# Performance work log

Hardware: AMD Instinct MI355X
Metric: run time of the kernel (lower is better)

## Reference

```python
import jax, jax.numpy as jnp
import numpy as np

K = 5          # number of spline bins
B = 5.0        # tail bound
HIDDEN = 8
MIN_W = 1e-3; MIN_H = 1e-3; MIN_D = 1e-3  # RQS defaults (Durkan et al.)


def setup_inputs() -> dict:
    n, d = 32768, 64
    L = d - 1
    P = 3 * K - 1
    ks = jax.random.split(jax.random.key(0), 8)
    x = jax.random.normal(ks[0], (n, d), jnp.float32) * 2.0
    init_param = jax.random.uniform(ks[1], (P,), jnp.float32, -0.5, 0.5)
    # ragged first layers: layer l (predicts dim l+1) sees x[:, :l+1]; zero-pad to width L
    mask = (jnp.arange(L)[None, :] <= jnp.arange(L)[:, None]).astype(jnp.float32)
    W1 = jax.random.normal(ks[2], (L, L, HIDDEN), jnp.float32) * 0.2 * mask[:, :, None]
    b1 = jax.random.normal(ks[3], (L, HIDDEN), jnp.float32) * 0.1
    W2 = jax.random.normal(ks[4], (L, HIDDEN, HIDDEN), jnp.float32) * 0.2
    b2 = jax.random.normal(ks[5], (L, HIDDEN), jnp.float32) * 0.1
    W3 = jax.random.normal(ks[6], (L, HIDDEN, P), jnp.float32) * 0.2
    b3 = jax.random.normal(ks[7], (L, P), jnp.float32) * 0.1
    return {"x": x, "init_param": init_param, "W1": W1, "b1": b1,
            "W2": W2, "b2": b2, "W3": W3, "b3": b3}


def _rqs(xf, Wu, Hu, Du):
    # xf: (M,), Wu/Hu: (M,K), Du: (M,K-1) -- vectorized unconstrained RQS, forward
    inside = (xf >= -B) & (xf <= B)
    const = float(np.log(np.exp(1.0 - MIN_D) - 1.0))
    Dpad = jnp.pad(Du, ((0, 0), (1, 1)), constant_values=const)

    widths = MIN_W + (1.0 - MIN_W * K) * jax.nn.softmax(Wu, axis=-1)
    cumw = jnp.pad(jnp.cumsum(widths, -1), ((0, 0), (1, 0)))
    cumw = 2.0 * B * cumw - B
    cumw = cumw.at[:, 0].set(-B).at[:, -1].set(B)
    widths = cumw[:, 1:] - cumw[:, :-1]

    heights = MIN_H + (1.0 - MIN_H * K) * jax.nn.softmax(Hu, axis=-1)
    cumh = jnp.pad(jnp.cumsum(heights, -1), ((0, 0), (1, 0)))
    cumh = 2.0 * B * cumh - B
    cumh = cumh.at[:, 0].set(-B).at[:, -1].set(B)
    heights = cumh[:, 1:] - cumh[:, :-1]

    derivs = MIN_D + jax.nn.softplus(Dpad)  # (M, K+1)

    xc = jnp.clip(xf, -B, B)
    idx = jnp.clip(jnp.sum(xc[:, None] >= cumw, axis=-1) - 1, 0, K - 1)
    take = lambda a: jnp.take_along_axis(a, idx[:, None], axis=-1)[:, 0]

    icw, ibw = take(cumw), take(widths)
    ich, ih = take(cumh), take(heights)
    idl = take(heights / widths)
    idv = take(derivs)
    idvp1 = take(derivs[:, 1:])

    theta = (xc - icw) / ibw
    tmt = theta * (1.0 - theta)
    num = ih * (idl * theta * theta + idv * tmt)
    den = idl + (idv + idvp1 - 2.0 * idl) * tmt
    out = ich + num / den
    dnum = idl * idl * (idvp1 * theta * theta + 2.0 * idl * tmt + idv * (1.0 - theta) ** 2)
    ld = jnp.log(dnum) - 2.0 * jnp.log(den)
    return jnp.where(inside, out, xf), jnp.where(inside, ld, 0.0)


def reference(x, init_param, W1, b1, W2, b2, W3, b3):
    n, d = x.shape
    L = d - 1
    P = 3 * K - 1
    # mask re-applied so padded W1 entries are exactly inert (ragged Linear(i, hidden))
    mask = (jnp.arange(L)[None, :] <= jnp.arange(L)[:, None]).astype(x.dtype)
    h = jnp.tanh(jnp.einsum('nj,ljh->lnh', x[:, :L], W1 * mask[:, :, None]) + b1[:, None, :])
    h = jnp.tanh(jnp.einsum('lnh,lhg->lng', h, W2) + b2[:, None, :])
    out = jnp.einsum('lng,lgp->lnp', h, W3) + b3[:, None, :]      # (L, n, P)
    p0 = jnp.broadcast_to(init_param, (1, n, P))                  # dim 0 uses init_param
    params = jnp.concatenate([p0, out], axis=0).reshape(d * n, P)  # dim-major, matches Ws layout
    Wu, Hu, Du = params[:, :K], params[:, K:2 * K], params[:, 2 * K:]
    xf = x.T.reshape(-1)  # x.transpose(0,1).flatten()
    zs, lds = _rqs(xf, Wu, Hu, Du)
    # NOTE: faithfully replicates the original's reshape of the dim-major flat
    # vector directly to (n, d) (as in the torch source).
    return zs.reshape(n, d), lds.reshape(n, d).sum(axis=1)
```

## Files before the change

### kernel.cpp

```cpp
#include <hip/hip_runtime.h>
#include <hip/hip_bf16.h>
#include <math.h>

#define KK 5
#define Bc 5.0f
#define NN 32768
#define DD 64
#define LL 63
#define PP 14
#define MIN_Wc 0.001f
#define MIN_Hc 0.001f
#define MIN_Dc 0.001f

typedef float f4 __attribute__((ext_vector_type(4)));
typedef float f32x4 __attribute__((ext_vector_type(4)));
typedef short short8 __attribute__((ext_vector_type(8)));

__device__ __forceinline__ float rcp_fast(float v)  { return __builtin_amdgcn_rcpf(v); }
__device__ __forceinline__ float exp_fast(float v)  { return __expf(v); }
__device__ __forceinline__ float log_fast(float v)  { return __logf(v); }
__device__ __forceinline__ float tanh_fast(float v) {
    float e = exp_fast(2.0f * v);
    return 1.0f - 2.0f * rcp_fast(e + 1.0f);
}
__device__ __forceinline__ float softplus_fast(float v) {
    return (v > 15.0f) ? v : log_fast(1.0f + exp_fast(v));
}
__device__ __forceinline__ ushort to_bf16u(float v) {
    __hip_bfloat16 b = __float2bfloat16(v);
    return *(ushort*)&b;
}

__global__ __launch_bounds__(256) void pack_b1(const float* __restrict__ W1,
                                               ushort* __restrict__ Bp) {
    int id = blockIdx.x * 256 + threadIdx.x;
    int n = id >> 6, k = id & 63;
    float v = 0.f;
    if (n < 504 && k < 63) {
        int l = n >> 3, h = n & 7;
        v = W1[(l * 63 + k) * 8 + h];
    }
    Bp[id] = to_bf16u(v);
}

#define AS 72
__global__ __launch_bounds__(256) void mlp1_kernel(
    const float* __restrict__ x, const ushort* __restrict__ Bp,
    const float* __restrict__ b1, ushort* __restrict__ h1out)
{
    __shared__ ushort Alds[64 * AS];
    __shared__ ushort Blds[128 * AS];
    const int tid = threadIdx.x;
    const int row0 = blockIdx.x * 64;
    const int nbase = blockIdx.y * 128;

    {
        int r = tid >> 2, c4 = (tid & 3) * 16;
        const f4* xg = (const f4*)(x + (size_t)(row0 + r) * 64 + c4);
        #pragma unroll
        for (int i = 0; i < 4; ++i) {
            f4 v = xg[i];
            ushort4 u;
            u.x = to_bf16u(v.x); u.y = to_bf16u(v.y);
            u.z = to_bf16u(v.z); u.w = to_bf16u(v.w);
            *(ushort4*)(&Alds[r * AS + c4 + i * 4]) = u;
        }
    }
    {
        const short8* src = (const short8*)(Bp + (size_t)nbase * 64);
        #pragma unroll
        for (int i = 0; i < 4; ++i) {
            int e = tid * 4 + i;
            int n = e >> 3, kc = (e & 7) * 8;
            *(short8*)(&Blds[n * AS + kc]) = src[e];
        }
    }
    __syncthreads();

    const int lane = tid & 63, wave = tid >> 6;
    const int m0 = wave * 16;
    const int qg = lane >> 4;
    const int ln = lane & 15;

    short8 a0 = *(const short8*)(&Alds[(m0 + ln) * AS + qg * 8]);
    short8 a1 = *(const short8*)(&Alds[(m0 + ln) * AS + 32 + qg * 8]);

    #pragma unroll
    for (int t = 0; t < 8; ++t) {
        short8 bf0 = *(const short8*)(&Blds[(t * 16 + ln) * AS + qg * 8]);
        short8 bf1 = *(const short8*)(&Blds[(t * 16 + ln) * AS + 32 + qg * 8]);
        f32x4 acc = {0.f, 0.f, 0.f, 0.f};
        acc = __builtin_amdgcn_mfma_f32_16x16x32_bf16(a0, bf0, acc, 0, 0, 0);
        acc = __builtin_amdgcn_mfma_f32_16x16x32_bf16(a1, bf1, acc, 0, 0, 0);

        int ng = nbase + t * 16 + ln;
        bool valid = ng < 504;
        float bias = valid ? b1[ng] : 0.f;
        int l = ng >> 3, h = ng & 7;
        ushort* dst = h1out + ((size_t)l * NN + row0 + m0 + qg * 4) * 8 + h;
        #pragma unroll
        for (int r = 0; r < 4; ++r) {
            float v = tanh_fast(acc[r] + bias);
            if (valid) dst[r * 8] = to_bf16u(v);
        }
    }
}

__global__ __launch_bounds__(256) void spline_kernel(
    const float* __restrict__ x, const float* __restrict__ init_param,
    const ushort* __restrict__ h1g,
    const float* __restrict__ W2, const float* __restrict__ b2,
    const float* __restrict__ W3, const float* __restrict__ b3,
    float* __restrict__ out)
{
    __shared__ float xs[64 * 65];
    const int s0 = blockIdx.x * 64;
    const int tid = threadIdx.x;
    for (int q = tid; q < 64 * 64; q += 256) {
        int r = q >> 6, c = q & 63;
        xs[r * 65 + c] = x[(size_t)(s0 + r) * 64 + c];
    }
    __syncthreads();

    const int lane = tid & 63, wave = tid >> 6;
    const int t = blockIdx.y * 4 + wave;

    #pragma unroll 1
    for (int kk = 0; kk < 4; ++kk) {
        int dd = __builtin_amdgcn_readfirstlane(t + kk * 16);

        float p[PP];
        if (dd == 0) {
            #pragma unroll
            for (int i = 0; i < PP; ++i) p[i] = init_param[i];
        } else {
            const int l = dd - 1;
            const uint4* hp = (const uint4*)(h1g + (size_t)l * NN * 8);
            uint4 hv = hp[s0 + lane];
            float h1f[8];
            h1f[0] = __uint_as_float(hv.x << 16);
            h1f[1] = __uint_as_float(hv.x & 0xFFFF0000u);
            h1f[2] = __uint_as_float(hv.y << 16);
            h1f[3] = __uint_as_float(hv.y & 0xFFFF0000u);
            h1f[4] = __uint_as_float(hv.z << 16);
            h1f[5] = __uint_as_float(hv.z & 0xFFFF0000u);
            h1f[6] = __uint_as_float(hv.w << 16);
            h1f[7] = __uint_as_float(hv.w & 0xFFFF0000u);

            float h2[8];
            #pragma unroll
            for (int g = 0; g < 8; ++g) h2[g] = b2[l * 8 + g];
            #pragma unroll
            for (int h = 0; h < 8; ++h) {
                #pragma unroll
                for (int g = 0; g < 8; ++g)
                    h2[g] = fmaf(h1f[h], W2[l * 64 + h * 8 + g], h2[g]);
            }
            #pragma unroll
            for (int g = 0; g < 8; ++g) h2[g] = tanh_fast(h2[g]);

            #pragma unroll
            for (int q = 0; q < PP; ++q) p[q] = b3[l * PP + q];
            #pragma unroll
            for (int g = 0; g < 8; ++g) {
                #pragma unroll
                for (int q = 0; q < PP; ++q)
                    p[q] = fmaf(h2[g], W3[(l * 8 + g) * PP + q], p[q]);
            }
        }

        const float xf = xs[lane * 65 + dd];

        float wmax = p[0];
        #pragma unroll
        for (int i = 1; i < KK; ++i) wmax = fmaxf(wmax, p[i]);
        float we[KK]; float wsum = 0.f;
        #pragma unroll
        for (int i = 0; i < KK; ++i) { we[i] = exp_fast(p[i] - wmax); wsum += we[i]; }
        const float wnorm = (1.0f - MIN_Wc * KK) * rcp_fast(wsum);
        float cumw[KK + 1], wdt[KK];
        cumw[0] = -Bc;
        float acw = 0.f;
        #pragma unroll
        for (int i = 0; i < KK; ++i) { acw += MIN_Wc + wnorm * we[i]; cumw[i + 1] = 2.f * Bc * acw - Bc; }
        cumw[KK] = Bc;
        #pragma unroll
        for (int i = 0; i < KK; ++i) wdt[i] = cumw[i + 1] - cumw[i];

        float hmax = p[KK];
        #pragma unroll
        for (int i = 1; i < KK; ++i) hmax = fmaxf(hmax, p[KK + i]);
        float he[KK]; float hsum = 0.f;
        #pragma unroll
        for (int i = 0; i < KK; ++i) { he[i] = exp_fast(p[KK + i] - hmax); hsum += he[i]; }
        const float hnorm = (1.0f - MIN_Hc * KK) * rcp_fast(hsum);
        float cumh[KK + 1], hgt[KK];
        cumh[0] = -Bc;
        float ach = 0.f;
        #pragma unroll
        for (int i = 0; i < KK; ++i) { ach += MIN_Hc + hnorm * he[i]; cumh[i + 1] = 2.f * Bc * ach - Bc; }
        cumh[KK] = Bc;
        #pragma unroll
        for (int i = 0; i < KK; ++i) hgt[i] = cumh[i + 1] - cumh[i];

        float derivs[KK + 1];
        derivs[0] = 1.0f;
        derivs[KK] = 1.0f;
        #pragma unroll
        for (int i = 0; i < KK - 1; ++i) derivs[i + 1] = MIN_Dc + softplus_fast(p[2 * KK + i]);

        const float xc = fminf(fmaxf(xf, -Bc), Bc);

        float icw = cumw[0], ibw = wdt[0], ich = cumh[0], ih = hgt[0];
        float idv = derivs[0], idvp1 = derivs[1];
        #pragma unroll
        for (int i = 1; i < KK; ++i) {
            bool c = xc >= cumw[i];
            icw   = c ? cumw[i]       : icw;
            ibw   = c ? wdt[i]        : ibw;
            ich   = c ? cumh[i]       : ich;
            ih    = c ? hgt[i]        : ih;
            idv   = c ? derivs[i]     : idv;
            idvp1 = c ? derivs[i + 1] : idvp1;
        }

        const float ibw_r = rcp_fast(ibw);
        const float idl = ih * ibw_r;
        const float theta = (xc - icw) * ibw_r;
        const float omt = 1.0f - theta;
        const float tmt = theta * omt;
        const float num = ih * (idl * theta * theta + idv * tmt);
        const float den = idl + (idv + idvp1 - 2.0f * idl) * tmt;
        const float outv = ich + num * rcp_fast(den);
        const float dnum = idl * idl * (idvp1 * theta * theta + 2.0f * idl * tmt + idv * omt * omt);
        const float ld = log_fast(dnum) - 2.0f * log_fast(den);

        const bool inside = (xf >= -Bc) && (xf <= Bc);
        const float z = inside ? outv : xf;
        float ldv = inside ? ld : 0.0f;

        out[dd * NN + s0 + lane] = z;

        #pragma unroll
        for (int off = 32; off > 0; off >>= 1) ldv += __shfl_down(ldv, off);
        if (lane == 0) out[NN * DD + dd * (NN / 64) + blockIdx.x] = ldv;
    }
}

extern "C" void kernel_launch(void* const* d_in, const int* in_sizes, int n_in,
                              void* d_out, int out_size, void* d_ws, size_t ws_size,
                              hipStream_t stream) {
    const float* x          = (const float*)d_in[0];
    const float* init_param = (const float*)d_in[1];
    const float* W1         = (const float*)d_in[2];
    const float* b1         = (const float*)d_in[3];
    const float* W2         = (const float*)d_in[4];
    const float* b2         = (const float*)d_in[5];
    const float* W3         = (const float*)d_in[6];
    const float* b3         = (const float*)d_in[7];
    float* out = (float*)d_out;

    ushort* Bp = (ushort*)d_ws;
    ushort* h1 = (ushort*)d_ws + 512 * 64;

    pack_b1<<<128, 256, 0, stream>>>(W1, Bp);
    mlp1_kernel<<<dim3(512, 4), 256, 0, stream>>>(x, Bp, b1, h1);
    spline_kernel<<<dim3(512, 4), 256, 0, stream>>>(x, init_param, h1,
                                                    W2, b2, W3, b3, out);
}
```

Before: 122.8 us.

## Fuse first-layer MFMA into spline kernel, keeping hidden activations in LDS

Merges the separate first-layer GEMM kernel and the spline kernel into one. Each block computes tanh(xW1+b1) for a chunk of 8 layers with MFMA, stages the bf16 results in a double-buffered LDS tile, then runs the layer-2/3 MLP and the spline on them. This removes the large global write and re-read of the hidden activations, plus one kernel launch. It also skips the second K-half MFMA for the lower half of the layers, where the triangular W1 mask makes those weights zero. In exchange the grid shrinks to 1024 blocks, LDS use per block rises, and B tiles are read straight from global memory with no LDS staging.

After: 117.1 us. -4.6%, faster.

```diff
diff --git a/kernel.cpp b/kernel.cpp
--- a/kernel.cpp
+++ b/kernel.cpp
@@ -43,207 +43,189 @@
     Bp[id] = to_bf16u(v);
 }
 
-#define AS 72
-__global__ __launch_bounds__(256) void mlp1_kernel(
-    const float* __restrict__ x, const ushort* __restrict__ Bp,
-    const float* __restrict__ b1, ushort* __restrict__ h1out)
-{
-    __shared__ ushort Alds[64 * AS];
-    __shared__ ushort Blds[128 * AS];
-    const int tid = threadIdx.x;
-    const int row0 = blockIdx.x * 64;
-    const int nbase = blockIdx.y * 128;
-
-    {
-        int r = tid >> 2, c4 = (tid & 3) * 16;
-        const f4* xg = (const f4*)(x + (size_t)(row0 + r) * 64 + c4);
-        #pragma unroll
-        for (int i = 0; i < 4; ++i) {
-            f4 v = xg[i];
-            ushort4 u;
-            u.x = to_bf16u(v.x); u.y = to_bf16u(v.y);
-            u.z = to_bf16u(v.z); u.w = to_bf16u(v.w);
-            *(ushort4*)(&Alds[r * AS + c4 + i * 4]) = u;
-        }
-    }
-    {
-        const short8* src = (const short8*)(Bp + (size_t)nbase * 64);
-        #pragma unroll
-        for (int i = 0; i < 4; ++i) {
-            int e = tid * 4 + i;
-            int n = e >> 3, kc = (e & 7) * 8;
-            *(short8*)(&Blds[n * AS + kc]) = src[e];
-        }
-    }
-    __syncthreads();
-
-    const int lane = tid & 63, wave = tid >> 6;
-    const int m0 = wave * 16;
-    const int qg = lane >> 4;
-    const int ln = lane & 15;
-
-    short8 a0 = *(const short8*)(&Alds[(m0 + ln) * AS + qg * 8]);
-    short8 a1 = *(const short8*)(&Alds[(m0 + ln) * AS + 32 + qg * 8]);
-
-    #pragma unroll
-    for (int t = 0; t < 8; ++t) {
-        short8 bf0 = *(const short8*)(&Blds[(t * 16 + ln) * AS + qg * 8]);
-        short8 bf1 = *(const short8*)(&Blds[(t * 16 + ln) * AS + 32 + qg * 8]);
-        f32x4 acc = {0.f, 0.f, 0.f, 0.f};
-        acc = __builtin_amdgcn_mfma_f32_16x16x32_bf16(a0, bf0, acc, 0, 0, 0);
-        acc = __builtin_amdgcn_mfma_f32_16x16x32_bf16(a1, bf1, acc, 0, 0, 0);
-
-        int ng = nbase + t * 16 + ln;
-        bool valid = ng < 504;
-        float bias = valid ? b1[ng] : 0.f;
-        int l = ng >> 3, h = ng & 7;
-        ushort* dst = h1out + ((size_t)l * NN + row0 + m0 + qg * 4) * 8 + h;
-        #pragma unroll
-        for (int r = 0; r < 4; ++r) {
-            float v = tanh_fast(acc[r] + bias);
-            if (valid) dst[r * 8] = to_bf16u(v);
-        }
-    }
-}
-
-__global__ __launch_bounds__(256) void spline_kernel(
+__device__ __forceinline__ short8 pack_a(f4 v0, f4 v1) {
+    short8 a;
+    a[0] = (short)to_bf16u(v0.x); a[1] = (short)to_bf16u(v0.y);
+    a[2] = (short)to_bf16u(v0.z); a[3] = (short)to_bf16u(v0.w);
+    a[4] = (short)to_bf16u(v1.x); a[5] = (short)to_bf16u(v1.y);
+    a[6] = (short)to_bf16u(v1.z); a[7] = (short)to_bf16u(v1.w);
+    return a;
+}
+
+__global__ __launch_bounds__(256) void fused_kernel(
     const float* __restrict__ x, const float* __restrict__ init_param,
-    const ushort* __restrict__ h1g,
+    const ushort* __restrict__ Bp, const float* __restrict__ b1,
     const float* __restrict__ W2, const float* __restrict__ b2,
     const float* __restrict__ W3, const float* __restrict__ b3,
     float* __restrict__ out)
 {
     __shared__ float xs[64 * 65];
+    __shared__ ushort h1c[2][64 * 72];
+    const int tid = threadIdx.x;
     const int s0 = blockIdx.x * 64;
-    const int tid = threadIdx.x;
+    const int y  = blockIdx.y;
+
     for (int q = tid; q < 64 * 64; q += 256) {
         int r = q >> 6, c = q & 63;
         xs[r * 65 + c] = x[(size_t)(s0 + r) * 64 + c];
     }
-    __syncthreads();
 
     const int lane = tid & 63, wave = tid >> 6;
-    const int t = blockIdx.y * 4 + wave;
-
+    const int ln = lane & 15, qg = lane >> 4;
+    const int m0 = wave * 16;
+
+    short8 a0, a1;
+    {
+        const float* xr = x + (size_t)(s0 + m0 + ln) * 64 + qg * 8;
+        a0 = pack_a(*(const f4*)xr, *(const f4*)(xr + 4));
+        if (y) a1 = pack_a(*(const f4*)(xr + 32), *(const f4*)(xr + 36));
+        else   a1 = a0;
+    }
+
+    int buf = 0;
     #pragma unroll 1
-    for (int kk = 0; kk < 4; ++kk) {
-        int dd = __builtin_amdgcn_readfirstlane(t + kk * 16);
-
-        float p[PP];
-        if (dd == 0) {
-            #pragma unroll
-            for (int i = 0; i < PP; ++i) p[i] = init_param[i];
-        } else {
-            const int l = dd - 1;
-            const uint4* hp = (const uint4*)(h1g + (size_t)l * NN * 8);
-            uint4 hv = hp[s0 + lane];
-            float h1f[8];
-            h1f[0] = __uint_as_float(hv.x << 16);
-            h1f[1] = __uint_as_float(hv.x & 0xFFFF0000u);
-            h1f[2] = __uint_as_float(hv.y << 16);
-            h1f[3] = __uint_as_float(hv.y & 0xFFFF0000u);
-            h1f[4] = __uint_as_float(hv.z << 16);
-            h1f[5] = __uint_as_float(hv.z & 0xFFFF0000u);
-            h1f[6] = __uint_as_float(hv.w << 16);
-            h1f[7] = __uint_as_float(hv.w & 0xFFFF0000u);
-
-            float h2[8];
-            #pragma unroll
-            for (int g = 0; g < 8; ++g) h2[g] = b2[l * 8 + g];
-            #pragma unroll
-            for (int h = 0; h < 8; ++h) {
-                #pragma unroll
-                for (int g = 0; g < 8; ++g)
-                    h2[g] = fmaf(h1f[h], W2[l * 64 + h * 8 + g], h2[g]);
-            }
-            #pragma unroll
-            for (int g = 0; g < 8; ++g) h2[g] = tanh_fast(h2[g]);
-
-            #pragma unroll
-            for (int q = 0; q < PP; ++q) p[q] = b3[l * PP + q];
-            #pragma unroll
-            for (int g = 0; g < 8; ++g) {
-                #pragma unroll
-                for (int q = 0; q < PP; ++q)
-                    p[q] = fmaf(h2[g], W3[(l * 8 + g) * PP + q], p[q]);
+    for (int c = 0; c < 4; ++c) {
+        const int gc = y * 4 + c;
+
+        #pragma unroll
+        for (int nt = 0; nt < 4; ++nt) {
+            int ncol = gc * 64 + nt * 16 + ln;
+            const short8* bp8 = (const short8*)(Bp + ncol * 64 + qg * 8);
+            f32x4 acc = {0.f, 0.f, 0.f, 0.f};
+            acc = __builtin_amdgcn_mfma_f32_16x16x32_bf16(a0, bp8[0], acc, 0, 0, 0);
+            if (y) acc = __builtin_amdgcn_mfma_f32_16x16x32_bf16(a1, bp8[4], acc, 0, 0, 0);
+            float bias = (ncol < 504) ? b1[ncol] : 0.f;
+            #pragma unroll
+            for (int r = 0; r < 4; ++r) {
+                float v = tanh_fast(acc[r] + bias);
+                h1c[buf][(m0 + qg * 4 + r) * 72 + nt * 16 + ln] = to_bf16u(v);
             }
         }
-
-        const float xf = xs[lane * 65 + dd];
-
-        float wmax = p[0];
-        #pragma unroll
-        for (int i = 1; i < KK; ++i) wmax = fmaxf(wmax, p[i]);
-        float we[KK]; float wsum = 0.f;
-        #pragma unroll
-        for (int i = 0; i < KK; ++i) { we[i] = exp_fast(p[i] - wmax); wsum += we[i]; }
-        const float wnorm = (1.0f - MIN_Wc * KK) * rcp_fast(wsum);
-        float cumw[KK + 1], wdt[KK];
-        cumw[0] = -Bc;
-        float acw = 0.f;
-        #pragma unroll
-        for (int i = 0; i < KK; ++i) { acw += MIN_Wc + wnorm * we[i]; cumw[i + 1] = 2.f * Bc * acw - Bc; }
-        cumw[KK] = Bc;
-        #pragma unroll
-        for (int i = 0; i < KK; ++i) wdt[i] = cumw[i + 1] - cumw[i];
-
-        float hmax = p[KK];
-        #pragma unroll
-        for (int i = 1; i < KK; ++i) hmax = fmaxf(hmax, p[KK + i]);
-        float he[KK]; float hsum = 0.f;
-        #pragma unroll
-        for (int i = 0; i < KK; ++i) { he[i] = exp_fast(p[KK + i] - hmax); hsum += he[i]; }
-        const float hnorm = (1.0f - MIN_Hc * KK) * rcp_fast(hsum);
-        float cumh[KK + 1], hgt[KK];
-        cumh[0] = -Bc;
-        float ach = 0.f;
-        #pragma unroll
-        for (int i = 0; i < KK; ++i) { ach += MIN_Hc + hnorm * he[i]; cumh[i + 1] = 2.f * Bc * ach - Bc; }
-        cumh[KK] = Bc;
-        #pragma unroll
-        for (int i = 0; i < KK; ++i) hgt[i] = cumh[i + 1] - cumh[i];
-
-        float derivs[KK + 1];
-        derivs[0] = 1.0f;
-        derivs[KK] = 1.0f;
-        #pragma unroll
-        for (int i = 0; i < KK - 1; ++i) derivs[i + 1] = MIN_Dc + softplus_fast(p[2 * KK + i]);
-
-        const float xc = fminf(fmaxf(xf, -Bc), Bc);
-
-        float icw = cumw[0], ibw = wdt[0], ich = cumh[0], ih = hgt[0];
-        float idv = derivs[0], idvp1 = derivs[1];
-        #pragma unroll
-        for (int i = 1; i < KK; ++i) {
-            bool c = xc >= cumw[i];
-            icw   = c ? cumw[i]       : icw;
-            ibw   = c ? wdt[i]        : ibw;
-            ich   = c ? cumh[i]       : ich;
-            ih    = c ? hgt[i]        : ih;
-            idv   = c ? derivs[i]     : idv;
-            idvp1 = c ? derivs[i + 1] : idvp1;
+        __syncthreads();
+
+        #pragma unroll 1
+        for (int it = 0; it < 2; ++it) {
+            int idx = wave * 2 + it;
+            int dd = (gc == 7 && idx == 7) ? 0 : gc * 8 + 1 + idx;
+            dd = __builtin_amdgcn_readfirstlane(dd);
+
+            float p[PP];
+            if (dd == 0) {
+                #pragma unroll
+                for (int i = 0; i < PP; ++i) p[i] = init_param[i];
+            } else {
+                const int l = dd - 1;
+                const int dl = l - gc * 8;
+                uint4 hv = *(const uint4*)&h1c[buf][lane * 72 + dl * 8];
+                float h1f[8];
+                h1f[0] = __uint_as_float(hv.x << 16);
+                h1f[1] = __uint_as_float(hv.x & 0xFFFF0000u);
+                h1f[2] = __uint_as_float(hv.y << 16);
+                h1f[3] = __uint_as_float(hv.y & 0xFFFF0000u);
+                h1f[4] = __uint_as_float(hv.z << 16);
+                h1f[5] = __uint_as_float(hv.z & 0xFFFF0000u);
+                h1f[6] = __uint_as_float(hv.w << 16);
+                h1f[7] = __uint_as_float(hv.w & 0xFFFF0000u);
+
+                float h2[8];
+                #pragma unroll
+                for (int g = 0; g < 8; ++g) h2[g] = b2[l * 8 + g];
+                #pragma unroll
+                for (int h = 0; h < 8; ++h) {
+                    #pragma unroll
+                    for (int g = 0; g < 8; ++g)
+                        h2[g] = fmaf(h1f[h], W2[l * 64 + h * 8 + g], h2[g]);
+                }
+                #pragma unroll
+                for (int g = 0; g < 8; ++g) h2[g] = tanh_fast(h2[g]);
+
+                #pragma unroll
+                for (int q = 0; q < PP; ++q) p[q] = b3[l * PP + q];
+                #pragma unroll
+                for (int g = 0; g < 8; ++g) {
+                    #pragma unroll
+                    for (int q = 0; q < PP; ++q)
+                        p[q] = fmaf(h2[g], W3[(l * 8 + g) * PP + q], p[q]);
+                }
+            }
+
+            const float xf = xs[lane * 65 + dd];
+
+            float wmax = p[0];
+            #pragma unroll
+            for (int i = 1; i < KK; ++i) wmax = fmaxf(wmax, p[i]);
+            float we[KK]; float wsum = 0.f;
+            #pragma unroll
+            for (int i = 0; i < KK; ++i) { we[i] = exp_fast(p[i] - wmax); wsum += we[i]; }
+            const float wnorm = (1.0f - MIN_Wc * KK) * rcp_fast(wsum);
+            float cumw[KK + 1], wdt[KK];
+            cumw[0] = -Bc;
+            float acw = 0.f;
+            #pragma unroll
+            for (int i = 0; i < KK; ++i) { acw += MIN_Wc + wnorm * we[i]; cumw[i + 1] = 2.f * Bc * acw - Bc; }
+            cumw[KK] = Bc;
+            #pragma unroll
+            for (int i = 0; i < KK; ++i) wdt[i] = cumw[i + 1] - cumw[i];
+
+            float hmax = p[KK];
+            #pragma unroll
+            for (int i = 1; i < KK; ++i) hmax = fmaxf(hmax, p[KK + i]);
+            float he[KK]; float hsum = 0.f;
+            #pragma unroll
+            for (int i = 0; i < KK; ++i) { he[i] = exp_fast(p[KK + i] - hmax); hsum += he[i]; }
+            const float hnorm = (1.0f - MIN_Hc * KK) * rcp_fast(hsum);
+            float cumh[KK + 1], hgt[KK];
+            cumh[0] = -Bc;
+            float ach = 0.f;
+            #pragma unroll
+            for (int i = 0; i < KK; ++i) { ach += MIN_Hc + hnorm * he[i]; cumh[i + 1] = 2.f * Bc * ach - Bc; }
+            cumh[KK] = Bc;
+            #pragma unroll
+            for (int i = 0; i < KK; ++i) hgt[i] = cumh[i + 1] - cumh[i];
+
+            float derivs[KK + 1];
+            derivs[0] = 1.0f;
+            derivs[KK] = 1.0f;
+            #pragma unroll
+            for (int i = 0; i < KK - 1; ++i) derivs[i + 1] = MIN_Dc + softplus_fast(p[2 * KK + i]);
+
+            const float xc = fminf(fmaxf(xf, -Bc), Bc);
+
+            float icw = cumw[0], ibw = wdt[0], ich = cumh[0], ih = hgt[0];
+            float idv = derivs[0], idvp1 = derivs[1];
+            #pragma unroll
+            for (int i = 1; i < KK; ++i) {
+                bool cc = xc >= cumw[i];
+                icw   = cc ? cumw[i]       : icw;
+                ibw   = cc ? wdt[i]        : ibw;
+                ich   = cc ? cumh[i]       : ich;
+                ih    = cc ? hgt[i]        : ih;
+                idv   = cc ? derivs[i]     : idv;
+                idvp1 = cc ? derivs[i + 1] : idvp1;
+            }
+
+            const float ibw_r = rcp_fast(ibw);
+            const float idl = ih * ibw_r;
+            const float theta = (xc - icw) * ibw_r;
+            const float omt = 1.0f - theta;
+            const float tmt = theta * omt;
+            const float num = ih * (idl * theta * theta + idv * tmt);
+            const float den = idl + (idv + idvp1 - 2.0f * idl) * tmt;
+            const float outv = ich + num * rcp_fast(den);
+            const float dnum = idl * idl * (idvp1 * theta * theta + 2.0f * idl * tmt + idv * omt * omt);
+            const float ld = log_fast(dnum) - 2.0f * log_fast(den);
+
+            const bool inside = (xf >= -Bc) && (xf <= Bc);
+            const float z = inside ? outv : xf;
+            float ldv = inside ? ld : 0.0f;
+
+            out[dd * NN + s0 + lane] = z;
+
+            #pragma unroll
+            for (int off = 32; off > 0; off >>= 1) ldv += __shfl_down(ldv, off);
+            if (lane == 0) out[NN * DD + dd * (NN / 64) + blockIdx.x] = ldv;
         }
-
-        const float ibw_r = rcp_fast(ibw);
-        const float idl = ih * ibw_r;
-        const float theta = (xc - icw) * ibw_r;
-        const float omt = 1.0f - theta;
-        const float tmt = theta * omt;
-        const float num = ih * (idl * theta * theta + idv * tmt);
-        const float den = idl + (idv + idvp1 - 2.0f * idl) * tmt;
-        const float outv = ich + num * rcp_fast(den);
-        const float dnum = idl * idl * (idvp1 * theta * theta + 2.0f * idl * tmt + idv * omt * omt);
-        const float ld = log_fast(dnum) - 2.0f * log_fast(den);
-
-        const bool inside = (xf >= -Bc) && (xf <= Bc);
-        const float z = inside ? outv : xf;
-        float ldv = inside ? ld : 0.0f;
-
-        out[dd * NN + s0 + lane] = z;
-
-        #pragma unroll
-        for (int off = 32; off > 0; off >>= 1) ldv += __shfl_down(ldv, off);
-        if (lane == 0) out[NN * DD + dd * (NN / 64) + blockIdx.x] = ldv;
+        buf ^= 1;
     }
 }
 
@@ -261,10 +243,8 @@
     float* out = (float*)d_out;
 
     ushort* Bp = (ushort*)d_ws;
-    ushort* h1 = (ushort*)d_ws + 512 * 64;
 
     pack_b1<<<128, 256, 0, stream>>>(W1, Bp);
-    mlp1_kernel<<<dim3(512, 4), 256, 0, stream>>>(x, Bp, b1, h1);
-    spline_kernel<<<dim3(512, 4), 256, 0, stream>>>(x, init_param, h1,
-                                                    W2, b2, W3, b3, out);
-}
+    fused_kernel<<<dim3(512, 2), 256, 0, stream>>>(x, init_param, Bp, b1,
+                                                   W2, b2, W3, b3, out);
+}
```
